# Performance work log

Measured on AMD Instinct MI355X. Metric: run time of the kernel, lower is better.

The kernel has to match this reference:

```python
import jax, jax.numpy as jnp
import numpy as np

N_SRC = 8192
N_DST = 8192
E = 524288
D = 128
M = 64


def layer_norm(x, g, b, eps=1e-5):
    mu = x.mean(-1, keepdims=True)
    var = ((x - mu) ** 2).mean(-1, keepdims=True)
    return (x - mu) * jax.lax.rsqrt(var + eps) * g + b


def setup_inputs() -> dict:
    key = jax.random.key(0)
    ks = jax.random.split(key, 32)

    def p(k, shape, s=0.02):
        return jax.random.normal(k, shape, jnp.float32) * s

    inp = {
        "src_embed": jax.random.normal(ks[0], (N_SRC, D), jnp.float32),
        "dst_embed": jax.random.normal(ks[1], (N_DST, D), jnp.float32),
        "v_s2d": jax.random.normal(ks[2], (E, M), jnp.float32),
        "v_d2s": jax.random.normal(ks[3], (E, M), jnp.float32),
        "e_s2d_dst": jax.random.randint(ks[4], (E,), 0, N_DST, jnp.int32),
        "e_d2s_dst": jax.random.randint(ks[5], (E,), 0, N_SRC, jnp.int32),
        # node transforms
        "W_src": p(ks[6], (D, D)), "b_src": jnp.zeros((D,), jnp.float32),
        "W_dst": p(ks[7], (D, D)), "b_dst": jnp.zeros((D,), jnp.float32),
        # edge-message transforms
        "W_sm": p(ks[8], (M, D)), "b_sm": jnp.zeros((D,), jnp.float32),
        "W_dm": p(ks[9], (M, D)), "b_dm": jnp.zeros((D,), jnp.float32),
        # apply_row: LNLayer (Linear+LayerNorm) then Linear
        "row_W1": p(ks[10], (D, D)), "row_b1": jnp.zeros((D,), jnp.float32),
        "row_g": jnp.ones((D,), jnp.float32), "row_beta": jnp.zeros((D,), jnp.float32),
        "row_W2": p(ks[11], (D, D)), "row_b2": jnp.zeros((D,), jnp.float32),
        # apply_col
        "col_W1": p(ks[12], (D, D)), "col_b1": jnp.zeros((D,), jnp.float32),
        "col_g": jnp.ones((D,), jnp.float32), "col_beta": jnp.zeros((D,), jnp.float32),
        "col_W2": p(ks[13], (D, D)), "col_b2": jnp.zeros((D,), jnp.float32),
    }
    return inp


def reference(src_embed, dst_embed, v_s2d, v_d2s, e_s2d_dst, e_d2s_dst,
              W_src, b_src, W_dst, b_dst, W_sm, b_sm, W_dm, b_dm,
              row_W1, row_b1, row_g, row_beta, row_W2, row_b2,
              col_W1, col_b1, col_g, col_beta, col_W2, col_b2):
    # node transforms: h[ntype]
    h_src = src_embed @ W_src + b_src          # [N_src, D]
    h_dst = dst_embed @ W_dst + b_dst          # [N_dst, D]
    # edge message transforms
    msg_s2d = v_s2d @ W_sm + b_sm              # [E, D]
    msg_d2s = v_d2s @ W_dm + b_dm              # [E, D]
    # message = h[dst-of-edge] * msg, scatter-sum onto destination nodes
    out_dst = jax.ops.segment_sum(h_dst[e_s2d_dst] * msg_s2d, e_s2d_dst,
                                  num_segments=N_DST)   # src2dst -> dst nodes
    out_src = jax.ops.segment_sum(h_src[e_d2s_dst] * msg_d2s, e_d2s_dst,
                                  num_segments=N_SRC)   # dst2src -> src nodes
    # residual apply: x + Linear(LayerNorm(Linear(out)))
    row = src_embed + (layer_norm(out_src @ row_W1 + row_b1, row_g, row_beta) @ row_W2 + row_b2)
    col = dst_embed + (layer_norm(out_dst @ col_W1 + col_b1, col_g, col_beta) @ col_W2 + col_b2)
    return row, col
```

## Files before the change

### kernel.cpp

```cpp
#include <hip/hip_runtime.h>


#define DEV __device__ __forceinline__

typedef __bf16 bf16x8 __attribute__((ext_vector_type(8)));
typedef unsigned short u16x8 __attribute__((ext_vector_type(8)));
typedef float f32x4 __attribute__((ext_vector_type(4)));

constexpr int N_NODES = 8192;
constexpr int NUM_E   = 524288;
constexpr int D       = 128;
constexpr int M       = 64;
constexpr int R       = 16;

DEV unsigned short f2bf(float f) {
    unsigned int x = __float_as_uint(f);
    unsigned int r = (x + 0x7fffu + ((x >> 16) & 1u)) >> 16;
    return (unsigned short)r;
}
DEV bf16x8 load8(const unsigned short* p) {
    return *reinterpret_cast<const bf16x8*>(p);
}
DEV bf16x8 cvt8(const float* p) {
    union { u16x8 u; bf16x8 b; } cv;
#pragma unroll
    for (int i = 0; i < 8; ++i) cv.u[i] = f2bf(p[i]);
    return cv.b;
}
DEV f32x4 mfma16(bf16x8 a, bf16x8 b, f32x4 c) {
    return __builtin_amdgcn_mfma_f32_16x16x32_bf16(a, b, c, 0, 0, 0);
}

struct TransArgs {
    const float* src[8];
    unsigned short* dst[8];
    int K[8];
};
__global__ __launch_bounds__(256) void transpose_k(TransArgs ta, int* __restrict__ counts) {
    int b = blockIdx.x;
    if (b >= 8) {
        int z = b - 8;
        int4 zero = {0, 0, 0, 0};
        int4* p = reinterpret_cast<int4*>(counts) + (size_t)z * 2048 + threadIdx.x;
#pragma unroll
        for (int q = 0; q < 8; ++q) p[q * 256] = zero;
        return;
    }
    const float* s = ta.src[b];
    unsigned short* d = ta.dst[b];
    int K = ta.K[b];
    int total = K << 7;
    for (int i = threadIdx.x; i < total; i += 256) {
        int k = i >> 7, n = i & 127;
        d[n * K + k] = f2bf(s[i]);
    }
}

__global__ __launch_bounds__(256) void hist_k(const int* __restrict__ i0,
                                              const int* __restrict__ i1,
                                              int* __restrict__ counts) {
    int t = blockIdx.x * 256 + threadIdx.x;
    int rep = blockIdx.x & (R - 1);
    int base = rep * N_NODES;
    const int4* p = (const int4*)i0;
    if (t >= NUM_E / 4) { p = (const int4*)i1; base += R * N_NODES; t -= NUM_E / 4; }
    int4 e = p[t];
    atomicAdd(counts + base + (e.x & (N_NODES - 1)), 1);
    atomicAdd(counts + base + (e.y & (N_NODES - 1)), 1);
    atomicAdd(counts + base + (e.z & (N_NODES - 1)), 1);
    atomicAdd(counts + base + (e.w & (N_NODES - 1)), 1);
}

__global__ __launch_bounds__(256) void scan_k(const int* __restrict__ counts,
                                              int* __restrict__ offsets,
                                              int* __restrict__ cursors,
                                              int* __restrict__ tot) {
    __shared__ int part[256];
    int t = threadIdx.x;
    int dir = blockIdx.x;
    const int* c = counts + (size_t)dir * R * N_NODES;
    int* off = offsets + dir * (N_NODES + 1);
    int* cur = cursors + (size_t)dir * R * N_NODES;
    int* tt = tot + dir * N_NODES;

    int sums[32];
#pragma unroll
    for (int i = 0; i < 32; ++i) sums[i] = 0;
    for (int r = 0; r < R; ++r) {
        const int4* p = (const int4*)(c + r * N_NODES + t * 32);
#pragma unroll
        for (int q = 0; q < 8; ++q) {
            int4 v = p[q];
            sums[q * 4 + 0] += v.x; sums[q * 4 + 1] += v.y;
            sums[q * 4 + 2] += v.z; sums[q * 4 + 3] += v.w;
        }
    }
    int local[32];
    int s = 0;
#pragma unroll
    for (int i = 0; i < 32; ++i) { local[i] = s; s += sums[i]; }
    part[t] = s;
    __syncthreads();
    for (int dd = 1; dd < 256; dd <<= 1) {
        int w = (t >= dd) ? part[t - dd] : 0;
        __syncthreads();
        part[t] += w;
        __syncthreads();
    }
    int base = part[t] - s;
#pragma unroll
    for (int i = 0; i < 32; ++i) {
        off[t * 32 + i] = base + local[i];
        tt[t * 32 + i] = sums[i];
    }
    if (t == 255) off[N_NODES] = part[255];
    int run[32];
#pragma unroll
    for (int i = 0; i < 32; ++i) run[i] = base + local[i];
    for (int r = 0; r < R; ++r) {
        const int4* p = (const int4*)(c + r * N_NODES + t * 32);
        int4* cp = (int4*)(cur + r * N_NODES + t * 32);
#pragma unroll
        for (int q = 0; q < 8; ++q) {
            int4 v = p[q];
            int4 w;
            w.x = run[q * 4 + 0]; w.y = run[q * 4 + 1];
            w.z = run[q * 4 + 2]; w.w = run[q * 4 + 3];
            cp[q] = w;
            run[q * 4 + 0] += v.x; run[q * 4 + 1] += v.y;
            run[q * 4 + 2] += v.z; run[q * 4 + 3] += v.w;
        }
    }
}

__global__ __launch_bounds__(256) void scatter_k(const int* __restrict__ i0,
                                                 const int* __restrict__ i1,
                                                 int* __restrict__ cursors,
                                                 int* __restrict__ csr) {
    int t = blockIdx.x * 256 + threadIdx.x;
    int rep = blockIdx.x & (R - 1);
    int dir = 0;
    if (t >= NUM_E / 4) { dir = 1; t -= NUM_E / 4; }
    const int4* idx = (const int4*)(dir ? i1 : i0);
    int4 nn = idx[t];
    int* cur = cursors + (size_t)dir * R * N_NODES + rep * N_NODES;
    int* c = csr + dir * NUM_E;
    int e = t * 4;
    c[atomicAdd(cur + (nn.x & (N_NODES - 1)), 1)] = e;
    c[atomicAdd(cur + (nn.y & (N_NODES - 1)), 1)] = e + 1;
    c[atomicAdd(cur + (nn.z & (N_NODES - 1)), 1)] = e + 2;
    c[atomicAdd(cur + (nn.w & (N_NODES - 1)), 1)] = e + 3;
}

__global__ __launch_bounds__(256) void gather_k(const float* __restrict__ v0,
                                                const float* __restrict__ v1,
                                                const int* __restrict__ offsets,
                                                const int* __restrict__ csr,
                                                unsigned short* __restrict__ Ab) {
    int gw = (blockIdx.x * 256 + threadIdx.x) >> 6;
    int dir = gw >> 13;
    int n = gw & (N_NODES - 1);
    const float* v = dir ? v1 : v0;
    const int* off = offsets + dir * (N_NODES + 1);
    const int* cs = csr + dir * NUM_E;
    unsigned short* A = Ab + (size_t)dir * N_NODES * M;

    int lane = threadIdx.x & 63;
    const int f16 = lane & 15;
    const int g = lane >> 4;
    int j0 = off[n], j1 = off[n + 1];
    f32x4 acc = {0.f, 0.f, 0.f, 0.f};

    int nfull = (j1 - j0) >> 4;
    int j = j0;
    if (nfull > 0) {
        int idx0 = cs[j + g], idx1 = cs[j + g + 4];
        int idx2 = cs[j + g + 8], idx3 = cs[j + g + 12];
        for (int it = 0; it < nfull; ++it) {
            int jn = j + 16;
            int p0 = 0, p1 = 0, p2 = 0, p3 = 0;
            if ((it + 1) < nfull) {
                p0 = cs[jn + g];
                p1 = cs[jn + g + 4];
                p2 = cs[jn + g + 8];
                p3 = cs[jn + g + 12];
            }
            f32x4 d0 = *(const f32x4*)(v + (size_t)idx0 * M + f16 * 4);
            f32x4 d1 = *(const f32x4*)(v + (size_t)idx1 * M + f16 * 4);
            f32x4 d2 = *(const f32x4*)(v + (size_t)idx2 * M + f16 * 4);
            f32x4 d3 = *(const f32x4*)(v + (size_t)idx3 * M + f16 * 4);
            acc += d0; acc += d1; acc += d2; acc += d3;
            idx0 = p0; idx1 = p1; idx2 = p2; idx3 = p3;
            j = jn;
        }
    }
    for (; j < j1; j += 4) {
        int e = j + g;
        if (e < j1) acc += *(const f32x4*)(v + (size_t)cs[e] * M + f16 * 4);
    }
#pragma unroll
    for (int i = 0; i < 4; ++i) {
        acc[i] += __shfl_xor(acc[i], 16, 64);
        acc[i] += __shfl_xor(acc[i], 32, 64);
    }
    if (g == 0) {
        union { unsigned short u[4]; unsigned long long ll; } w;
#pragma unroll
        for (int i = 0; i < 4; ++i) w.u[i] = f2bf(acc[i]);
        *reinterpret_cast<unsigned long long*>(A + (size_t)n * M + f16 * 4) = w.ll;
    }
}

struct SideArgs {
    const float* X;
    const unsigned short* Wnode_t;
    const float* bnode;
    const unsigned short* Abf;
    const int* counts;
    const unsigned short* Wmsg_t;
    const float* bmsg;
    const unsigned short* W1_t;
    const float* b1;
    const float* g;
    const float* beta;
    const unsigned short* W2_t;
    const float* b2;
    float* out;
};

__global__ __launch_bounds__(256) void apply_k(SideArgs A0, SideArgs A1) {
    const int side = blockIdx.x >> 9;
    const SideArgs& a = side ? A1 : A0;
    const int grp = blockIdx.x & 511;
    const int nb = grp * 16;
    const int w = threadIdx.x >> 6;
    const int lane = threadIdx.x & 63;
    const int m = lane & 15;
    const int quad = lane >> 4;

    __shared__ __align__(16) unsigned short sP[16 * 136];
    __shared__ float part_s[4][16], part_sq[4][16];

    bf16x8 af[4];
#pragma unroll
    for (int ks = 0; ks < 4; ++ks)
        af[ks] = cvt8(a.X + (size_t)(nb + m) * D + ks * 32 + quad * 8);
    f32x4 acc_h[2] = {{0.f, 0.f, 0.f, 0.f}, {0.f, 0.f, 0.f, 0.f}};
#pragma unroll
    for (int i = 0; i < 2; ++i) {
        int dt = 2 * w + i;
#pragma unroll
        for (int ks = 0; ks < 4; ++ks) {
            bf16x8 bfr = load8(a.Wnode_t + (size_t)(dt * 16 + m) * D + ks * 32 + quad * 8);
            acc_h[i] = mfma16(af[ks], bfr, acc_h[i]);
        }
    }
    bf16x8 at[2];
#pragma unroll
    for (int ks = 0; ks < 2; ++ks)
        at[ks] = load8(a.Abf + (size_t)(nb + m) * M + ks * 32 + quad * 8);
    f32x4 acc_t[2] = {{0.f, 0.f, 0.f, 0.f}, {0.f, 0.f, 0.f, 0.f}};
#pragma unroll
    for (int i = 0; i < 2; ++i) {
        int dt = 2 * w + i;
#pragma unroll
        for (int ks = 0; ks < 2; ++ks) {
            bf16x8 bfr = load8(a.Wmsg_t + (size_t)(dt * 16 + m) * M + ks * 32 + quad * 8);
            acc_t[i] = mfma16(at[ks], bfr, acc_t[i]);
        }
    }
    {
        float cnt_f[4];
#pragma unroll
        for (int r = 0; r < 4; ++r) cnt_f[r] = (float)a.counts[nb + quad * 4 + r];
#pragma unroll
        for (int i = 0; i < 2; ++i) {
            int dt = 2 * w + i;
            float bn = a.bnode[dt * 16 + m];
            float bm = a.bmsg[dt * 16 + m];
#pragma unroll
            for (int r = 0; r < 4; ++r) {
                float hv = acc_h[i][r] + bn;
                float tv = acc_t[i][r] + cnt_f[r] * bm;
                sP[(quad * 4 + r) * 136 + dt * 16 + m] = f2bf(hv * tv);
            }
        }
    }
    __syncthreads();
    bf16x8 au[4];
#pragma unroll
    for (int ks = 0; ks < 4; ++ks)
        au[ks] = load8(sP + m * 136 + ks * 32 + quad * 8);
    f32x4 acc_u[2] = {{0.f, 0.f, 0.f, 0.f}, {0.f, 0.f, 0.f, 0.f}};
#pragma unroll
    for (int i = 0; i < 2; ++i) {
        int dt = 2 * w + i;
#pragma unroll
        for (int ks = 0; ks < 4; ++ks) {
            bf16x8 bfr = load8(a.W1_t + (size_t)(dt * 16 + m) * D + ks * 32 + quad * 8);
            acc_u[i] = mfma16(au[ks], bfr, acc_u[i]);
        }
    }
    float g_f[2], beta_f[2];
#pragma unroll
    for (int i = 0; i < 2; ++i) {
        int dt = 2 * w + i;
        float b1v = a.b1[dt * 16 + m];
        g_f[i] = a.g[dt * 16 + m];
        beta_f[i] = a.beta[dt * 16 + m];
#pragma unroll
        for (int r = 0; r < 4; ++r) acc_u[i][r] += b1v;
    }
    float s[4], sq[4];
#pragma unroll
    for (int r = 0; r < 4; ++r) { s[r] = 0.f; sq[r] = 0.f; }
#pragma unroll
    for (int i = 0; i < 2; ++i)
#pragma unroll
        for (int r = 0; r < 4; ++r) { float u = acc_u[i][r]; s[r] += u; sq[r] += u * u; }
#pragma unroll
    for (int off = 1; off < 16; off <<= 1) {
#pragma unroll
        for (int r = 0; r < 4; ++r) {
            s[r] += __shfl_xor(s[r], off, 64);
            sq[r] += __shfl_xor(sq[r], off, 64);
        }
    }
    if (m == 0) {
#pragma unroll
        for (int r = 0; r < 4; ++r) {
            part_s[w][quad * 4 + r] = s[r];
            part_sq[w][quad * 4 + r] = sq[r];
        }
    }
    __syncthreads();
    float mu[4], rstd[4];
#pragma unroll
    for (int r = 0; r < 4; ++r) {
        int node = quad * 4 + r;
        float S = part_s[0][node] + part_s[1][node] + part_s[2][node] + part_s[3][node];
        float SQ = part_sq[0][node] + part_sq[1][node] + part_sq[2][node] + part_sq[3][node];
        mu[r] = S * (1.0f / 128.0f);
        float var = SQ * (1.0f / 128.0f) - mu[r] * mu[r];
        rstd[r] = rsqrtf(fmaxf(var, 0.f) + 1e-5f);
    }
#pragma unroll
    for (int i = 0; i < 2; ++i) {
        int dt = 2 * w + i;
#pragma unroll
        for (int r = 0; r < 4; ++r) {
            float ln = (acc_u[i][r] - mu[r]) * rstd[r] * g_f[i] + beta_f[i];
            sP[(quad * 4 + r) * 136 + dt * 16 + m] = f2bf(ln);
        }
    }
    __syncthreads();
    bf16x8 ay[4];
#pragma unroll
    for (int ks = 0; ks < 4; ++ks)
        ay[ks] = load8(sP + m * 136 + ks * 32 + quad * 8);
    f32x4 acc_y[2] = {{0.f, 0.f, 0.f, 0.f}, {0.f, 0.f, 0.f, 0.f}};
#pragma unroll
    for (int i = 0; i < 2; ++i) {
        int dt = 2 * w + i;
#pragma unroll
        for (int ks = 0; ks < 4; ++ks) {
            bf16x8 bfr = load8(a.W2_t + (size_t)(dt * 16 + m) * D + ks * 32 + quad * 8);
            acc_y[i] = mfma16(ay[ks], bfr, acc_y[i]);
        }
    }
#pragma unroll
    for (int i = 0; i < 2; ++i) {
        int dt = 2 * w + i;
        float b2v = a.b2[dt * 16 + m];
#pragma unroll
        for (int r = 0; r < 4; ++r) {
            int node = nb + quad * 4 + r;
            int d = dt * 16 + m;
            float xv = a.X[(size_t)node * D + d];
            a.out[(size_t)node * D + d] = acc_y[i][r] + b2v + xv;
        }
    }
}

extern "C" void kernel_launch(void* const* d_in, const int* in_sizes, int n_in,
                              void* d_out, int out_size, void* d_ws, size_t ws_size,
                              hipStream_t stream) {
    const float* src_embed = (const float*)d_in[0];
    const float* dst_embed = (const float*)d_in[1];
    const float* v_s2d = (const float*)d_in[2];
    const float* v_d2s = (const float*)d_in[3];
    const int* e_s2d = (const int*)d_in[4];
    const int* e_d2s = (const int*)d_in[5];
    const float* W_src = (const float*)d_in[6];
    const float* b_src = (const float*)d_in[7];
    const float* W_dst = (const float*)d_in[8];
    const float* b_dst = (const float*)d_in[9];
    const float* W_sm = (const float*)d_in[10];
    const float* b_sm = (const float*)d_in[11];
    const float* W_dm = (const float*)d_in[12];
    const float* b_dm = (const float*)d_in[13];
    const float* row_W1 = (const float*)d_in[14];
    const float* row_b1 = (const float*)d_in[15];
    const float* row_g = (const float*)d_in[16];
    const float* row_beta = (const float*)d_in[17];
    const float* row_W2 = (const float*)d_in[18];
    const float* row_b2 = (const float*)d_in[19];
    const float* col_W1 = (const float*)d_in[20];
    const float* col_b1 = (const float*)d_in[21];
    const float* col_g = (const float*)d_in[22];
    const float* col_beta = (const float*)d_in[23];
    const float* col_W2 = (const float*)d_in[24];
    const float* col_b2 = (const float*)d_in[25];
    float* out = (float*)d_out;

    char* ws = (char*)d_ws;
    int* counts = (int*)(ws + 0);
    int* offsets = (int*)(ws + 1048576);
    int* cursors = (int*)(ws + 1114368);
    int* tot = (int*)(ws + 2162944);
    unsigned short* Wt = (unsigned short*)(ws + 2228480);
    unsigned short* Abf = (unsigned short*)(ws + 2457856);
    int* csr = (int*)(out + (size_t)N_NODES * D);

    TransArgs ta;
    const float* srcs[8] = {W_src, W_dst, W_sm, W_dm, row_W1, row_W2, col_W1, col_W2};
    int Ks[8] = {128, 128, 64, 64, 128, 128, 128, 128};
    int offs[8] = {0, 16384, 32768, 40960, 49152, 65536, 81920, 98304};
    for (int i = 0; i < 8; ++i) { ta.src[i] = srcs[i]; ta.dst[i] = Wt + offs[i]; ta.K[i] = Ks[i]; }
    transpose_k<<<40, 256, 0, stream>>>(ta, counts);

    hist_k<<<(2 * NUM_E / 4) / 256, 256, 0, stream>>>(e_s2d, e_d2s, counts);
    scan_k<<<2, 256, 0, stream>>>(counts, offsets, cursors, tot);
    scatter_k<<<(2 * NUM_E / 4) / 256, 256, 0, stream>>>(e_s2d, e_d2s, cursors, csr);

    gather_k<<<(2 * N_NODES * 64) / 256, 256, 0, stream>>>(
        v_s2d, v_d2s, offsets, csr, Abf);

    SideArgs rowA = {src_embed, Wt + 0, b_src, Abf + (size_t)N_NODES * M, tot + N_NODES,
                     Wt + 40960, b_dm, Wt + 49152, row_b1, row_g, row_beta, Wt + 65536, row_b2,
                     out};
    SideArgs colA = {dst_embed, Wt + 16384, b_dst, Abf, tot,
                     Wt + 32768, b_sm, Wt + 81920, col_b1, col_g, col_beta, Wt + 98304, col_b2,
                     out + (size_t)N_NODES * D};
    apply_k<<<1024, 256, 0, stream>>>(rowA, colA);
}
```

Measured before the change: 524.2 us.

## Split count scan into parallel per-node reduce and unroll gather loop deeper

The replica count reduction and cursor computation move out of the 2-block scan into a separate reduce kernel that runs across many blocks and writes per-replica relative cursors. The scan then only prefix-sums the per-node totals, and scatter adds the node offset to the relative cursor. The gather loop now handles 32 edges per iteration with 8 outstanding loads, plus a 16-edge tail, to raise memory-level parallelism. The cost is an extra kernel launch and an extra offset read per edge in scatter.

After: 467.7 us. -10.8%, faster.

```diff
diff --git a/kernel.cpp b/kernel.cpp
--- a/kernel.cpp
+++ b/kernel.cpp
@@ -71,34 +71,35 @@
     atomicAdd(counts + base + (e.w & (N_NODES - 1)), 1);
 }
 
-__global__ __launch_bounds__(256) void scan_k(const int* __restrict__ counts,
-                                              int* __restrict__ offsets,
-                                              int* __restrict__ cursors,
-                                              int* __restrict__ tot) {
+__global__ __launch_bounds__(256) void reduce_k(const int* __restrict__ counts,
+                                                int* __restrict__ cur_rel,
+                                                int* __restrict__ tot) {
+    int n = blockIdx.x * 256 + threadIdx.x;
+    int dir = n >> 13;
+    int node = n & (N_NODES - 1);
+    const int* c = counts + (size_t)dir * R * N_NODES + node;
+    int* cr = cur_rel + (size_t)dir * R * N_NODES + node;
+    int s = 0;
+#pragma unroll
+    for (int r = 0; r < R; ++r) {
+        int v = c[r * N_NODES];
+        cr[r * N_NODES] = s;
+        s += v;
+    }
+    tot[n] = s;
+}
+
+__global__ __launch_bounds__(256) void scan_k(const int* __restrict__ tot,
+                                              int* __restrict__ offsets) {
     __shared__ int part[256];
     int t = threadIdx.x;
     int dir = blockIdx.x;
-    const int* c = counts + (size_t)dir * R * N_NODES;
+    const int* tt = tot + dir * N_NODES;
     int* off = offsets + dir * (N_NODES + 1);
-    int* cur = cursors + (size_t)dir * R * N_NODES;
-    int* tt = tot + dir * N_NODES;
-
-    int sums[32];
-#pragma unroll
-    for (int i = 0; i < 32; ++i) sums[i] = 0;
-    for (int r = 0; r < R; ++r) {
-        const int4* p = (const int4*)(c + r * N_NODES + t * 32);
-#pragma unroll
-        for (int q = 0; q < 8; ++q) {
-            int4 v = p[q];
-            sums[q * 4 + 0] += v.x; sums[q * 4 + 1] += v.y;
-            sums[q * 4 + 2] += v.z; sums[q * 4 + 3] += v.w;
-        }
-    }
     int local[32];
     int s = 0;
 #pragma unroll
-    for (int i = 0; i < 32; ++i) { local[i] = s; s += sums[i]; }
+    for (int i = 0; i < 32; ++i) { int v = tt[t * 32 + i]; local[i] = s; s += v; }
     part[t] = s;
     __syncthreads();
     for (int dd = 1; dd < 256; dd <<= 1) {
@@ -109,33 +110,14 @@
     }
     int base = part[t] - s;
 #pragma unroll
-    for (int i = 0; i < 32; ++i) {
-        off[t * 32 + i] = base + local[i];
-        tt[t * 32 + i] = sums[i];
-    }
+    for (int i = 0; i < 32; ++i) off[t * 32 + i] = base + local[i];
     if (t == 255) off[N_NODES] = part[255];
-    int run[32];
-#pragma unroll
-    for (int i = 0; i < 32; ++i) run[i] = base + local[i];
-    for (int r = 0; r < R; ++r) {
-        const int4* p = (const int4*)(c + r * N_NODES + t * 32);
-        int4* cp = (int4*)(cur + r * N_NODES + t * 32);
-#pragma unroll
-        for (int q = 0; q < 8; ++q) {
-            int4 v = p[q];
-            int4 w;
-            w.x = run[q * 4 + 0]; w.y = run[q * 4 + 1];
-            w.z = run[q * 4 + 2]; w.w = run[q * 4 + 3];
-            cp[q] = w;
-            run[q * 4 + 0] += v.x; run[q * 4 + 1] += v.y;
-            run[q * 4 + 2] += v.z; run[q * 4 + 3] += v.w;
-        }
-    }
 }
 
 __global__ __launch_bounds__(256) void scatter_k(const int* __restrict__ i0,
                                                  const int* __restrict__ i1,
-                                                 int* __restrict__ cursors,
+                                                 const int* __restrict__ offsets,
+                                                 int* __restrict__ cur_rel,
                                                  int* __restrict__ csr) {
     int t = blockIdx.x * 256 + threadIdx.x;
     int rep = blockIdx.x & (R - 1);
@@ -143,13 +125,16 @@
     if (t >= NUM_E / 4) { dir = 1; t -= NUM_E / 4; }
     const int4* idx = (const int4*)(dir ? i1 : i0);
     int4 nn = idx[t];
-    int* cur = cursors + (size_t)dir * R * N_NODES + rep * N_NODES;
+    const int* off = offsets + dir * (N_NODES + 1);
+    int* cr = cur_rel + (size_t)dir * R * N_NODES + rep * N_NODES;
     int* c = csr + dir * NUM_E;
     int e = t * 4;
-    c[atomicAdd(cur + (nn.x & (N_NODES - 1)), 1)] = e;
-    c[atomicAdd(cur + (nn.y & (N_NODES - 1)), 1)] = e + 1;
-    c[atomicAdd(cur + (nn.z & (N_NODES - 1)), 1)] = e + 2;
-    c[atomicAdd(cur + (nn.w & (N_NODES - 1)), 1)] = e + 3;
+    int a = nn.x & (N_NODES - 1), b = nn.y & (N_NODES - 1);
+    int cc = nn.z & (N_NODES - 1), d = nn.w & (N_NODES - 1);
+    c[off[a] + atomicAdd(cr + a, 1)] = e;
+    c[off[b] + atomicAdd(cr + b, 1)] = e + 1;
+    c[off[cc] + atomicAdd(cr + cc, 1)] = e + 2;
+    c[off[d] + atomicAdd(cr + d, 1)] = e + 3;
 }
 
 __global__ __launch_bounds__(256) void gather_k(const float* __restrict__ v0,
@@ -169,30 +154,47 @@
     const int f16 = lane & 15;
     const int g = lane >> 4;
     int j0 = off[n], j1 = off[n + 1];
+    int rem = j1 - j0;
     f32x4 acc = {0.f, 0.f, 0.f, 0.f};
 
-    int nfull = (j1 - j0) >> 4;
+    int nfull = rem >> 5;
     int j = j0;
     if (nfull > 0) {
-        int idx0 = cs[j + g], idx1 = cs[j + g + 4];
-        int idx2 = cs[j + g + 8], idx3 = cs[j + g + 12];
+        int ia[8];
+#pragma unroll
+        for (int q = 0; q < 8; ++q) ia[q] = cs[j + g + q * 4];
         for (int it = 0; it < nfull; ++it) {
-            int jn = j + 16;
-            int p0 = 0, p1 = 0, p2 = 0, p3 = 0;
+            int jn = j + 32;
+            int pa[8];
             if ((it + 1) < nfull) {
-                p0 = cs[jn + g];
-                p1 = cs[jn + g + 4];
-                p2 = cs[jn + g + 8];
-                p3 = cs[jn + g + 12];
+#pragma unroll
+                for (int q = 0; q < 8; ++q) pa[q] = cs[jn + g + q * 4];
+            } else {
+#pragma unroll
+                for (int q = 0; q < 8; ++q) pa[q] = 0;
             }
-            f32x4 d0 = *(const f32x4*)(v + (size_t)idx0 * M + f16 * 4);
-            f32x4 d1 = *(const f32x4*)(v + (size_t)idx1 * M + f16 * 4);
-            f32x4 d2 = *(const f32x4*)(v + (size_t)idx2 * M + f16 * 4);
-            f32x4 d3 = *(const f32x4*)(v + (size_t)idx3 * M + f16 * 4);
-            acc += d0; acc += d1; acc += d2; acc += d3;
-            idx0 = p0; idx1 = p1; idx2 = p2; idx3 = p3;
+            f32x4 d[8];
+#pragma unroll
+            for (int q = 0; q < 8; ++q)
+                d[q] = *(const f32x4*)(v + (size_t)ia[q] * M + f16 * 4);
+#pragma unroll
+            for (int q = 0; q < 8; ++q) acc += d[q];
+#pragma unroll
+            for (int q = 0; q < 8; ++q) ia[q] = pa[q];
             j = jn;
         }
+    }
+    if (rem & 16) {
+        int ia[4];
+#pragma unroll
+        for (int q = 0; q < 4; ++q) ia[q] = cs[j + g + q * 4];
+        f32x4 d[4];
+#pragma unroll
+        for (int q = 0; q < 4; ++q)
+            d[q] = *(const f32x4*)(v + (size_t)ia[q] * M + f16 * 4);
+#pragma unroll
+        for (int q = 0; q < 4; ++q) acc += d[q];
+        j += 16;
     }
     for (; j < j1; j += 4) {
         int e = j + g;
@@ -416,7 +418,7 @@
     char* ws = (char*)d_ws;
     int* counts = (int*)(ws + 0);
     int* offsets = (int*)(ws + 1048576);
-    int* cursors = (int*)(ws + 1114368);
+    int* cur_rel = (int*)(ws + 1114368);
     int* tot = (int*)(ws + 2162944);
     unsigned short* Wt = (unsigned short*)(ws + 2228480);
     unsigned short* Abf = (unsigned short*)(ws + 2457856);
@@ -430,8 +432,9 @@
     transpose_k<<<40, 256, 0, stream>>>(ta, counts);
 
     hist_k<<<(2 * NUM_E / 4) / 256, 256, 0, stream>>>(e_s2d, e_d2s, counts);
-    scan_k<<<2, 256, 0, stream>>>(counts, offsets, cursors, tot);
-    scatter_k<<<(2 * NUM_E / 4) / 256, 256, 0, stream>>>(e_s2d, e_d2s, cursors, csr);
+    reduce_k<<<(2 * N_NODES) / 256, 256, 0, stream>>>(counts, cur_rel, tot);
+    scan_k<<<2, 256, 0, stream>>>(tot, offsets);
+    scatter_k<<<(2 * NUM_E / 4) / 256, 256, 0, stream>>>(e_s2d, e_d2s, offsets, cur_rel, csr);
 
     gather_k<<<(2 * N_NODES * 64) / 256, 256, 0, stream>>>(
         v_s2d, v_d2s, offsets, csr, Abf);
```
